# Kernel optimization log

Hardware: AMD Instinct MI355X
Metric: run time of the kernel (lower is better)

The kernel has to match this reference:

```python
import jax, jax.numpy as jnp
import numpy as np

H = 12          # num_attention_heads
D = 768         # hidden_size
HD = D // H     # attention_head_size = 64
B, S = 2, 4096
NEG = -1e9

def setup_inputs() -> dict:
    key = jax.random.key(0)
    ks = jax.random.split(key, 6)
    scale = 0.02
    inp = {
        'x': jax.random.normal(ks[0], (B, S, D), jnp.float32),
        'mask': jax.random.randint(ks[1], (B, 1, 1, S), 0, 2, jnp.int32),
        'Wq': jax.random.normal(ks[2], (D, D), jnp.float32) * scale,
        'bq': jnp.zeros((D,), jnp.float32),
        'Wk': jax.random.normal(ks[3], (D, D), jnp.float32) * scale,
        'bk': jnp.zeros((D,), jnp.float32),
        'Wv': jax.random.normal(ks[4], (D, D), jnp.float32) * scale,
        'bv': jnp.zeros((D,), jnp.float32),
        'Wo': jax.random.normal(ks[5], (D, D), jnp.float32) * scale,
        'bo': jnp.zeros((D,), jnp.float32),
    }
    return inp

def reference(x, mask, Wq, bq, Wk, bk, Wv, bv, Wo, bo):
    b, s, _ = x.shape
    # QKV projections (torch Linear: y = x @ W^T + b)
    q = (x @ Wq.T + bq).reshape(b, s, H, HD).transpose(0, 2, 1, 3)  # [B,H,S,HD]
    k = (x @ Wk.T + bk).reshape(b, s, H, HD).transpose(0, 2, 1, 3)
    v = (x @ Wv.T + bv).reshape(b, s, H, HD).transpose(0, 2, 1, 3)
    scores = jnp.einsum('bhqd,bhkd->bhqk', q, k) / jnp.sqrt(jnp.float32(HD))
    scores = jnp.where(mask == 0, jnp.float32(NEG), scores)
    attn = jax.nn.softmax(scores, axis=-1)  # dropout is identity in eval
    ctx = jnp.einsum('bhqk,bhkd->bhqd', attn, v)
    ctx = ctx.transpose(0, 2, 1, 3).reshape(b, s, D)
    return ctx @ Wo.T + bo
```

## Files before the change

kernel.cpp:

```cpp
#include <hip/hip_runtime.h>


#define S_LEN 4096
#define NHEAD 12
#define NEGB2 (-1.442695e9f)
#define THR2 11.541561f
#define QSCALE 0.18033688f

typedef __attribute__((ext_vector_type(8))) short short8;
typedef __attribute__((ext_vector_type(4))) float f32x4;
typedef __attribute__((ext_vector_type(4))) int i32x4;

__device__ __forceinline__ unsigned short f2bf(float f) {
  unsigned u = __builtin_bit_cast(unsigned, f);
  u += 0x7fffu + ((u >> 16) & 1u);
  return (unsigned short)(u >> 16);
}

__device__ __forceinline__ f32x4 mfma_bf16(short8 a, short8 b, f32x4 c) {
  return __builtin_amdgcn_mfma_f32_16x16x32_bf16(a, b, c, 0, 0, 0);
}

__device__ __forceinline__ void gload16(const void* g, void* l) {
  __builtin_amdgcn_global_load_lds(
      (const __attribute__((address_space(1))) void*)g,
      (__attribute__((address_space(3))) void*)l, 16, 0, 0);
}

__global__ __launch_bounds__(64) void mask_scan(const int* __restrict__ mask,
                                                int* __restrict__ pos,
                                                int* __restrict__ cnt) {
  const int b = blockIdx.x;
  const int lane = threadIdx.x;
  const int* mb = mask + b * S_LEN;
  int* pb = pos + b * S_LEN;
  const int base = lane * 64;
  int cntl = 0;
  for (int j = 0; j < 64; j++) cntl += (mb[base + j] != 0);
  int x = cntl;
#pragma unroll
  for (int off = 1; off < 64; off <<= 1) {
    int y = __shfl_up(x, off);
    if (lane >= off) x += y;
  }
  const int total = __shfl(x, 63);
  int o = x - cntl;
  for (int j = 0; j < 64; j++) {
    const int mv = mb[base + j];
    pb[base + j] = (mv != 0) ? o : -1;
    o += (mv != 0);
  }
  if (lane == 0) cnt[b] = total;
}

__global__ __launch_bounds__(256) void cvt_kernel(const float* __restrict__ in,
                                                  unsigned short* __restrict__ out,
                                                  int n8) {
  int i = blockIdx.x * blockDim.x + threadIdx.x;
  int stride = gridDim.x * blockDim.x;
  for (; i < n8; i += stride) {
    float4 a = ((const float4*)in)[i * 2];
    float4 b = ((const float4*)in)[i * 2 + 1];
    short8 r;
    r[0] = (short)f2bf(a.x); r[1] = (short)f2bf(a.y);
    r[2] = (short)f2bf(a.z); r[3] = (short)f2bf(a.w);
    r[4] = (short)f2bf(b.x); r[5] = (short)f2bf(b.y);
    r[6] = (short)f2bf(b.z); r[7] = (short)f2bf(b.w);
    ((short8*)out)[i] = r;
  }
}

__global__ __launch_bounds__(256) void cvt_w4_kernel(const float* __restrict__ w0,
                                                     const float* __restrict__ w1,
                                                     const float* __restrict__ w2,
                                                     const float* __restrict__ w3,
                                                     unsigned short* __restrict__ out,
                                                     int n8) {
  const int k = blockIdx.y;
  const float* in = (k == 0) ? w0 : (k == 1) ? w1 : (k == 2) ? w2 : w3;
  unsigned short* dst = out + (size_t)k * n8 * 8;
  int i = blockIdx.x * blockDim.x + threadIdx.x;
  int stride = gridDim.x * blockDim.x;
  for (; i < n8; i += stride) {
    float4 a = ((const float4*)in)[i * 2];
    float4 b = ((const float4*)in)[i * 2 + 1];
    short8 r;
    r[0] = (short)f2bf(a.x); r[1] = (short)f2bf(a.y);
    r[2] = (short)f2bf(a.z); r[3] = (short)f2bf(a.w);
    r[4] = (short)f2bf(b.x); r[5] = (short)f2bf(b.y);
    r[6] = (short)f2bf(b.z); r[7] = (short)f2bf(b.w);
    ((short8*)dst)[i] = r;
  }
}

template <int EPI>
__global__ __launch_bounds__(256)
void gemm_bt(const unsigned short* __restrict__ A, const unsigned short* __restrict__ Bm,
             int K,
             const float* __restrict__ bias0, const float* __restrict__ bias1,
             const float* __restrict__ bias2, const int* __restrict__ pos,
             unsigned short* __restrict__ qkv_out, float* __restrict__ f_out) {
  __shared__ short As[2][128][32];
  __shared__ short Bs[2][128][32];
  const int n0 = blockIdx.x * 128;
  const int m0 = blockIdx.y * 128;
  const int t = threadIdx.x;
  const int lane = t & 63;
  const int w = t >> 6, wm = w >> 1, wn = w & 1;
  const int c = lane & 15, g = lane >> 4;
  const int srow = t >> 2, sch = t & 3;

  f32x4 acc[4][4] = {};
  const int nk = K >> 5;

#define G_STAGE(bsel, kt)                                                     \
  {                                                                           \
    _Pragma("unroll") for (int p = 0; p < 2; p++) {                           \
      const int row = p * 64 + srow;                                          \
      const int gcol = (kt) + ((sch ^ ((row >> 1) & 3)) * 8);                 \
      gload16(A + (size_t)(m0 + row) * K + gcol,                              \
              (char*)&As[bsel][0][0] + p * 4096 + (t >> 6) * 1024);           \
      gload16(Bm + (size_t)(n0 + row) * K + gcol,                             \
              (char*)&Bs[bsel][0][0] + p * 4096 + (t >> 6) * 1024);           \
    }                                                                         \
  }

  G_STAGE(0, 0);
  for (int kt = 0; kt < nk; kt++) {
    const int cur = kt & 1;
    __syncthreads();
    if (kt + 1 < nk) G_STAGE(cur ^ 1, (kt + 1) << 5);
    const int sw = (c >> 1) & 3;
    short8 af[4], bfr[4];
#pragma unroll
    for (int i = 0; i < 4; i++) {
      af[i]  = *(const short8*)&As[cur][wm * 64 + i * 16 + c][(g ^ sw) * 8];
      bfr[i] = *(const short8*)&Bs[cur][wn * 64 + i * 16 + c][(g ^ sw) * 8];
    }
#pragma unroll
    for (int mi = 0; mi < 4; mi++)
#pragma unroll
      for (int ni = 0; ni < 4; ni++)
        acc[mi][ni] = mfma_bf16(af[mi], bfr[ni], acc[mi][ni]);
  }
#undef G_STAGE

  if constexpr (EPI == 0) {
    const int tix = n0 / 768;
    const float* bias = (tix == 0) ? bias0 : (tix == 1) ? bias1 : bias2;
    unsigned short* dst = qkv_out + tix * (2 * NHEAD * S_LEN * 64);
    if (tix == 0) {
#pragma unroll
      for (int mi = 0; mi < 4; mi++) {
        const int r0 = m0 + wm * 64 + mi * 16 + (g << 2);
#pragma unroll
        for (int ni = 0; ni < 4; ni++) {
          const int jr = n0 + wn * 64 + ni * 16 + c;
          const int h = jr >> 6, d = jr & 63;
          const float bv = bias[jr];
#pragma unroll
          for (int reg = 0; reg < 4; reg++) {
            const int r = r0 + reg;
            const int b = r >> 12, s = r & (S_LEN - 1);
            dst[(((b * NHEAD + h) * S_LEN + s) << 6) + d] =
                f2bf((acc[mi][ni][reg] + bv) * QSCALE);
          }
        }
      }
    } else if (tix == 1) {
#pragma unroll
      for (int mi = 0; mi < 4; mi++) {
        const int r0 = m0 + wm * 64 + mi * 16 + (g << 2);
#pragma unroll
        for (int reg = 0; reg < 4; reg++) {
          const int r = r0 + reg;
          const int b = r >> 12, s = r & (S_LEN - 1);
          const int cpos = pos[b * S_LEN + s];
          if (cpos >= 0) {
#pragma unroll
            for (int ni = 0; ni < 4; ni++) {
              const int jr = (n0 - 768) + wn * 64 + ni * 16 + c;
              const int h = jr >> 6, d = jr & 63;
              dst[(((b * NHEAD + h) * S_LEN + cpos) << 6) + d] =
                  f2bf(acc[mi][ni][reg] + bias[jr]);
            }
          }
        }
      }
    } else {
#pragma unroll
      for (int mi = 0; mi < 4; mi++) {
        const int r0 = m0 + wm * 64 + mi * 16 + (g << 2);
#pragma unroll
        for (int reg = 0; reg < 4; reg++) {
          const int r = r0 + reg;
          const int b = r >> 12, s = r & (S_LEN - 1);
          const int cpos = pos[b * S_LEN + s];
          if (cpos >= 0) {
#pragma unroll
            for (int ni = 0; ni < 4; ni++) {
              const int jr = (n0 - 1536) + wn * 64 + ni * 16 + c;
              const int h = jr >> 6, d = jr & 63;
              dst[((size_t)((b * NHEAD + h) * 64 + d) << 12) + cpos] =
                  f2bf(acc[mi][ni][reg] + bias[jr]);
            }
          }
        }
      }
    }
  } else {
#pragma unroll
    for (int mi = 0; mi < 4; mi++) {
      const int r0 = m0 + wm * 64 + mi * 16 + (g << 2);
#pragma unroll
      for (int ni = 0; ni < 4; ni++) {
        const int gc = n0 + wn * 64 + ni * 16 + c;
        const float bv = bias0[gc];
#pragma unroll
        for (int reg = 0; reg < 4; reg++)
          f_out[(r0 + reg) * 768 + gc] = acc[mi][ni][reg] + bv;
      }
    }
  }
}

__global__ __launch_bounds__(256)
void attn_kernel(const unsigned short* __restrict__ Q, const unsigned short* __restrict__ Km,
                 const unsigned short* __restrict__ Vtg, const int* __restrict__ cnt,
                 unsigned short* __restrict__ ctx) {
  __shared__ short Ks[2][64][64];
  __shared__ short Vt[2][64][64];
  const int qt = blockIdx.x;
  const int bh = blockIdx.y;
  const int b = bh / NHEAD, h = bh % NHEAD;
  const unsigned short* Qb = Q + bh * (S_LEN * 64);
  const unsigned short* Kb = Km + bh * (S_LEN * 64);
  const unsigned short* Vb = Vtg + (size_t)bh * 64 * S_LEN;
  const int t = threadIdx.x, lane = t & 63, w = t >> 6;
  const int c = lane & 15, g = lane >> 4;
  const int q0 = qt * 128 + w * 32;
  const int cntb = cnt[b];
  const int ntiles = (cntb + 63) >> 6;
  const bool lo32 = (lane < 32);

  short8 qf[2][2];
#pragma unroll
  for (int qi = 0; qi < 2; qi++)
#pragma unroll
    for (int kk = 0; kk < 2; kk++)
      qf[qi][kk] = *(const short8*)(Qb + (q0 + qi * 16 + c) * 64 + kk * 32 + g * 8);

  f32x4 oacc[4][2] = {};
  float mrun[2], lrun[2];
  mrun[0] = mrun[1] = -__builtin_inff();
  lrun[0] = lrun[1] = 0.f;

  const int srow = t >> 3, sch = t & 7;

#define A_STAGE(bsel, k0v)                                                    \
  {                                                                           \
    _Pragma("unroll") for (int p = 0; p < 2; p++) {                           \
      const int row = p * 32 + srow;                                          \
      const int gc8 = ((sch ^ (row & 7)) * 8);                                \
      gload16(Kb + (size_t)((k0v) + row) * 64 + gc8,                          \
              (char*)&Ks[bsel][0][0] + p * 4096 + (t >> 6) * 1024);           \
      gload16(Vb + (size_t)row * S_LEN + (k0v) + gc8,                         \
              (char*)&Vt[bsel][0][0] + p * 4096 + (t >> 6) * 1024);           \
    }                                                                         \
  }

  A_STAGE(0, 0);

  for (int it = 0; it < ntiles; ++it) {
    const int bd = it & 1;
    const int k0 = it * 64;
    __syncthreads();
    if (it + 1 < ntiles) A_STAGE(bd ^ 1, k0 + 64);

    f32x4 st[2][4];
    __builtin_amdgcn_s_setprio(1);
#pragma unroll
    for (int mi = 0; mi < 4; mi++) {
      short8 ka0 = *(const short8*)&Ks[bd][mi * 16 + c][(g ^ (c & 7)) * 8];
      short8 ka1 = *(const short8*)&Ks[bd][mi * 16 + c][((4 + g) ^ (c & 7)) * 8];
#pragma unroll
      for (int qi = 0; qi < 2; qi++) {
        f32x4 zz = {0.f, 0.f, 0.f, 0.f};
        zz = mfma_bf16(ka0, qf[qi][0], zz);
        zz = mfma_bf16(ka1, qf[qi][1], zz);
        st[qi][mi] = zz;
      }
    }
    __builtin_amdgcn_s_setprio(0);
    if (k0 + 64 > cntb) {
#pragma unroll
      for (int mi = 0; mi < 4; mi++)
#pragma unroll
        for (int r = 0; r < 4; r++) {
          const float pb = (k0 + 16 * mi + 4 * g + r >= cntb) ? NEGB2 : 0.f;
          st[0][mi][r] += pb;
          st[1][mi][r] += pb;
        }
    }
    float pm[2];
#pragma unroll
    for (int qi = 0; qi < 2; qi++) {
      float x = st[qi][0][0];
#pragma unroll
      for (int mi = 0; mi < 4; mi++)
#pragma unroll
        for (int r = 0; r < 4; r++) x = fmaxf(x, st[qi][mi][r]);
      x = fmaxf(x, __shfl_xor(x, 16));
      x = fmaxf(x, __shfl_xor(x, 32));
      pm[qi] = x;
    }
    if (!__all((pm[0] <= mrun[0] + THR2) && (pm[1] <= mrun[1] + THR2))) {
#pragma unroll
      for (int qi = 0; qi < 2; qi++) {
        float mnew = fmaxf(mrun[qi], pm[qi]);
        float al = __builtin_amdgcn_exp2f(mrun[qi] - mnew);
        mrun[qi] = mnew;
        lrun[qi] *= al;
#pragma unroll
        for (int dmi = 0; dmi < 4; dmi++)
#pragma unroll
          for (int r = 0; r < 4; r++) oacc[dmi][qi][r] *= al;
      }
    }
    unsigned uu[2][4][2];
#pragma unroll
    for (int qi = 0; qi < 2; qi++) {
      float ps = 0.f;
#pragma unroll
      for (int mi = 0; mi < 4; mi++)
#pragma unroll
        for (int r = 0; r < 4; r++) {
          float p = __builtin_amdgcn_exp2f(st[qi][mi][r] - mrun[qi]);
          st[qi][mi][r] = p;
          ps += p;
        }
      ps += __shfl_xor(ps, 16);
      ps += __shfl_xor(ps, 32);
      lrun[qi] += ps;
#pragma unroll
      for (int mi = 0; mi < 4; mi++) {
        asm("v_cvt_pk_bf16_f32 %0, %1, %2"
            : "=v"(uu[qi][mi][0]) : "v"(st[qi][mi][0]), "v"(st[qi][mi][1]));
        asm("v_cvt_pk_bf16_f32 %0, %1, %2"
            : "=v"(uu[qi][mi][1]) : "v"(st[qi][mi][2]), "v"(st[qi][mi][3]));
      }
    }
#pragma unroll
    for (int kk = 0; kk < 2; kk++) {
      short8 pb[2];
#pragma unroll
      for (int qi = 0; qi < 2; qi++) {
        i32x4 dw;
#pragma unroll
        for (int x = 0; x < 2; x++) {
          unsigned pa = uu[qi][2 * kk][x], qa = pa;
          asm("v_permlane32_swap_b32 %0, %1" : "+v"(pa), "+v"(qa));
          asm("v_permlane16_swap_b32 %0, %1" : "+v"(pa), "+v"(qa));
          unsigned pbr = uu[qi][2 * kk + 1][x], qbr = pbr;
          asm("v_permlane32_swap_b32 %0, %1" : "+v"(pbr), "+v"(qbr));
          asm("v_permlane16_swap_b32 %0, %1" : "+v"(pbr), "+v"(qbr));
          dw[x]     = (int)(lo32 ? pa : pbr);
          dw[2 + x] = (int)(lo32 ? qa : qbr);
        }
        pb[qi] = __builtin_bit_cast(short8, dw);
      }
      __builtin_amdgcn_s_setprio(1);
#pragma unroll
      for (int dmi = 0; dmi < 4; dmi++) {
        short8 vf = *(const short8*)&Vt[bd][16 * dmi + c][((4 * kk + g) ^ (c & 7)) * 8];
        oacc[dmi][0] = mfma_bf16(vf, pb[0], oacc[dmi][0]);
        oacc[dmi][1] = mfma_bf16(vf, pb[1], oacc[dmi][1]);
      }
      __builtin_amdgcn_s_setprio(0);
    }
  }
#undef A_STAGE
#pragma unroll
  for (int qi = 0; qi < 2; qi++) {
    const float inv = 1.f / lrun[qi];
    const int row = q0 + qi * 16 + c;
#pragma unroll
    for (int dmi = 0; dmi < 4; dmi++) {
      float x0 = oacc[dmi][qi][0] * inv, x1 = oacc[dmi][qi][1] * inv;
      float x2 = oacc[dmi][qi][2] * inv, x3 = oacc[dmi][qi][3] * inv;
      unsigned p0, p1;
      asm("v_cvt_pk_bf16_f32 %0, %1, %2" : "=v"(p0) : "v"(x0), "v"(x1));
      asm("v_cvt_pk_bf16_f32 %0, %1, %2" : "=v"(p1) : "v"(x2), "v"(x3));
      uint2 u2v; u2v.x = p0; u2v.y = p1;
      *(uint2*)&ctx[(size_t)(b * S_LEN + row) * 768 + h * 64 + 16 * dmi + 4 * g] = u2v;
    }
  }
}

extern "C" void kernel_launch(void* const* d_in, const int* in_sizes, int n_in,
                              void* d_out, int out_size, void* d_ws, size_t ws_size,
                              hipStream_t stream) {
  const float* x  = (const float*)d_in[0];
  const int* mask = (const int*)d_in[1];
  const float* Wq = (const float*)d_in[2];
  const float* bq = (const float*)d_in[3];
  const float* Wk = (const float*)d_in[4];
  const float* bk = (const float*)d_in[5];
  const float* Wv = (const float*)d_in[6];
  const float* bv = (const float*)d_in[7];
  const float* Wo = (const float*)d_in[8];
  const float* bo = (const float*)d_in[9];
  float* out = (float*)d_out;

  const int NE = 8192 * 768;
  const int WE = 768 * 768;
  unsigned short* ws   = (unsigned short*)d_ws;
  unsigned short* xb   = ws;
  unsigned short* wqkv = xb + NE;
  unsigned short* wob  = wqkv + 3 * WE;
  unsigned short* qb   = wob + WE;
  unsigned short* ctxb = qb + 3 * NE;
  int* pos = (int*)(ctxb + NE);
  int* cnt = pos + 2 * S_LEN;

  mask_scan<<<dim3(2), 64, 0, stream>>>(mask, pos, cnt);
  cvt_kernel<<<dim3(2048), 256, 0, stream>>>(x, xb, NE / 8);
  cvt_w4_kernel<<<dim3(288, 4), 256, 0, stream>>>(Wq, Wk, Wv, Wo, wqkv, WE / 8);

  gemm_bt<0><<<dim3(18, 64), 256, 0, stream>>>(xb, wqkv, 768, bq, bk, bv, pos,
                                               qb, nullptr);
  attn_kernel<<<dim3(32, 24), 256, 0, stream>>>(qb, qb + NE, qb + 2 * NE, cnt, ctxb);
  gemm_bt<1><<<dim3(6, 64), 256, 0, stream>>>(ctxb, wob, 768, bo, nullptr, nullptr,
                                              nullptr, nullptr, out);
}
```

Measured before the change: 299.1 us.

## Store V row-major and transpose it into LDS inside the attention kernel

```diff
diff --git a/kernel.cpp b/kernel.cpp
--- a/kernel.cpp
+++ b/kernel.cpp
@@ -167,7 +167,7 @@
           }
         }
       }
-    } else if (tix == 1) {
+    } else {
 #pragma unroll
       for (int mi = 0; mi < 4; mi++) {
         const int r0 = m0 + wm * 64 + mi * 16 + (g << 2);
@@ -179,7 +179,7 @@
           if (cpos >= 0) {
 #pragma unroll
             for (int ni = 0; ni < 4; ni++) {
-              const int jr = (n0 - 768) + wn * 64 + ni * 16 + c;
+              const int jr = (n0 - tix * 768) + wn * 64 + ni * 16 + c;
               const int h = jr >> 6, d = jr & 63;
               dst[(((b * NHEAD + h) * S_LEN + cpos) << 6) + d] =
                   f2bf(acc[mi][ni][reg] + bias[jr]);
@@ -187,26 +187,6 @@
           }
         }
       }
-    } else {
-#pragma unroll
-      for (int mi = 0; mi < 4; mi++) {
-        const int r0 = m0 + wm * 64 + mi * 16 + (g << 2);
-#pragma unroll
-        for (int reg = 0; reg < 4; reg++) {
-          const int r = r0 + reg;
-          const int b = r >> 12, s = r & (S_LEN - 1);
-          const int cpos = pos[b * S_LEN + s];
-          if (cpos >= 0) {
-#pragma unroll
-            for (int ni = 0; ni < 4; ni++) {
-              const int jr = (n0 - 1536) + wn * 64 + ni * 16 + c;
-              const int h = jr >> 6, d = jr & 63;
-              dst[((size_t)((b * NHEAD + h) * 64 + d) << 12) + cpos] =
-                  f2bf(acc[mi][ni][reg] + bias[jr]);
-            }
-          }
-        }
-      }
     }
   } else {
 #pragma unroll
@@ -226,16 +206,16 @@
 
 __global__ __launch_bounds__(256)
 void attn_kernel(const unsigned short* __restrict__ Q, const unsigned short* __restrict__ Km,
-                 const unsigned short* __restrict__ Vtg, const int* __restrict__ cnt,
+                 const unsigned short* __restrict__ V, const int* __restrict__ cnt,
                  unsigned short* __restrict__ ctx) {
   __shared__ short Ks[2][64][64];
-  __shared__ short Vt[2][64][64];
+  __shared__ short Vt[2][64][72];
   const int qt = blockIdx.x;
   const int bh = blockIdx.y;
   const int b = bh / NHEAD, h = bh % NHEAD;
   const unsigned short* Qb = Q + bh * (S_LEN * 64);
   const unsigned short* Kb = Km + bh * (S_LEN * 64);
-  const unsigned short* Vb = Vtg + (size_t)bh * 64 * S_LEN;
+  const unsigned short* Vb = V + bh * (S_LEN * 64);
   const int t = threadIdx.x, lane = t & 63, w = t >> 6;
   const int c = lane & 15, g = lane >> 4;
   const int q0 = qt * 128 + w * 32;
@@ -256,26 +236,39 @@
   lrun[0] = lrun[1] = 0.f;
 
   const int srow = t >> 3, sch = t & 7;
-
-#define A_STAGE(bsel, k0v)                                                    \
+  const int swzw = sch << 3;
+
+#define K_STAGE(bsel, k0v)                                                    \
   {                                                                           \
     _Pragma("unroll") for (int p = 0; p < 2; p++) {                           \
       const int row = p * 32 + srow;                                          \
       const int gc8 = ((sch ^ (row & 7)) * 8);                                \
       gload16(Kb + (size_t)((k0v) + row) * 64 + gc8,                          \
               (char*)&Ks[bsel][0][0] + p * 4096 + (t >> 6) * 1024);           \
-      gload16(Vb + (size_t)row * S_LEN + (k0v) + gc8,                         \
-              (char*)&Vt[bsel][0][0] + p * 4096 + (t >> 6) * 1024);           \
     }                                                                         \
   }
 
-  A_STAGE(0, 0);
+  K_STAGE(0, 0);
+  {
+    short8 v0a = *(const short8*)(Vb + (size_t)srow * 64 + sch * 8);
+    short8 v1a = *(const short8*)(Vb + (size_t)(srow + 32) * 64 + sch * 8);
+#pragma unroll
+    for (int j = 0; j < 8; j++) {
+      Vt[0][sch * 8 + j][srow ^ swzw] = v0a[j];
+      Vt[0][sch * 8 + j][(srow + 32) ^ swzw] = v1a[j];
+    }
+  }
 
   for (int it = 0; it < ntiles; ++it) {
     const int bd = it & 1;
     const int k0 = it * 64;
     __syncthreads();
-    if (it + 1 < ntiles) A_STAGE(bd ^ 1, k0 + 64);
+    short8 nv0, nv1;
+    if (it + 1 < ntiles) {
+      K_STAGE(bd ^ 1, k0 + 64);
+      nv0 = *(const short8*)(Vb + (size_t)(k0 + 64 + srow) * 64 + sch * 8);
+      nv1 = *(const short8*)(Vb + (size_t)(k0 + 64 + srow + 32) * 64 + sch * 8);
+    }
 
     f32x4 st[2][4];
     __builtin_amdgcn_s_setprio(1);
@@ -305,11 +298,15 @@
     float pm[2];
 #pragma unroll
     for (int qi = 0; qi < 2; qi++) {
-      float x = st[qi][0][0];
-#pragma unroll
-      for (int mi = 0; mi < 4; mi++)
-#pragma unroll
-        for (int r = 0; r < 4; r++) x = fmaxf(x, st[qi][mi][r]);
+      float a0 = fmaxf(fmaxf(st[qi][0][0], st[qi][0][1]),
+                       fmaxf(st[qi][0][2], st[qi][0][3]));
+      float a1 = fmaxf(fmaxf(st[qi][1][0], st[qi][1][1]),
+                       fmaxf(st[qi][1][2], st[qi][1][3]));
+      float a2 = fmaxf(fmaxf(st[qi][2][0], st[qi][2][1]),
+                       fmaxf(st[qi][2][2], st[qi][2][3]));
+      float a3 = fmaxf(fmaxf(st[qi][3][0], st[qi][3][1]),
+                       fmaxf(st[qi][3][2], st[qi][3][3]));
+      float x = fmaxf(fmaxf(a0, a1), fmaxf(a2, a3));
       x = fmaxf(x, __shfl_xor(x, 16));
       x = fmaxf(x, __shfl_xor(x, 32));
       pm[qi] = x;
@@ -330,15 +327,15 @@
     unsigned uu[2][4][2];
 #pragma unroll
     for (int qi = 0; qi < 2; qi++) {
-      float ps = 0.f;
-#pragma unroll
-      for (int mi = 0; mi < 4; mi++)
-#pragma unroll
-        for (int r = 0; r < 4; r++) {
-          float p = __builtin_amdgcn_exp2f(st[qi][mi][r] - mrun[qi]);
-          st[qi][mi][r] = p;
-          ps += p;
-        }
+      float s4[4];
+#pragma unroll
+      for (int mi = 0; mi < 4; mi++) {
+#pragma unroll
+        for (int r = 0; r < 4; r++)
+          st[qi][mi][r] = __builtin_amdgcn_exp2f(st[qi][mi][r] - mrun[qi]);
+        s4[mi] = (st[qi][mi][0] + st[qi][mi][1]) + (st[qi][mi][2] + st[qi][mi][3]);
+      }
+      float ps = (s4[0] + s4[1]) + (s4[2] + s4[3]);
       ps += __shfl_xor(ps, 16);
       ps += __shfl_xor(ps, 32);
       lrun[qi] += ps;
@@ -372,14 +369,22 @@
       __builtin_amdgcn_s_setprio(1);
 #pragma unroll
       for (int dmi = 0; dmi < 4; dmi++) {
-        short8 vf = *(const short8*)&Vt[bd][16 * dmi + c][((4 * kk + g) ^ (c & 7)) * 8];
+        const int hsw = ((2 * dmi + (c >> 3)) & 7) << 3;
+        short8 vf = *(const short8*)&Vt[bd][16 * dmi + c][(32 * kk + 8 * g) ^ hsw];
         oacc[dmi][0] = mfma_bf16(vf, pb[0], oacc[dmi][0]);
         oacc[dmi][1] = mfma_bf16(vf, pb[1], oacc[dmi][1]);
       }
       __builtin_amdgcn_s_setprio(0);
     }
-  }
-#undef A_STAGE
+    if (it + 1 < ntiles) {
+#pragma unroll
+      for (int j = 0; j < 8; j++) {
+        Vt[bd ^ 1][sch * 8 + j][srow ^ swzw] = nv0[j];
+        Vt[bd ^ 1][sch * 8 + j][(srow + 32) ^ swzw] = nv1[j];
+      }
+    }
+  }
+#undef K_STAGE
 #pragma unroll
   for (int qi = 0; qi < 2; qi++) {
     const float inv = 1.f / lrun[qi];
```

Measured after the change: 296.8 us. About the same (-0.8%).
